# Kernel tuning notes

Measured on AMD Instinct MI355X. Metric: run time of the kernel, lower is better.

## Reference

```python
import jax, jax.numpy as jnp
import numpy as np

N_NODES = 100000
N_EDGES = 600000
IN_C, HID_C, OUT_C = 128, 128, 64


def setup_inputs() -> dict:
    key = jax.random.key(0)
    k1, k2, k3, k4 = jax.random.split(key, 4)
    x = jax.random.normal(k1, (N_NODES, IN_C), dtype=jnp.float32)
    edge_index = jax.random.randint(k2, (2, N_EDGES), 0, N_NODES, dtype=jnp.int64)
    # Glorot-ish init for linear weights
    W1 = jax.random.normal(k3, (IN_C, HID_C), dtype=jnp.float32) / np.sqrt(IN_C)
    b1 = jnp.zeros((HID_C,), dtype=jnp.float32)
    W2 = jax.random.normal(k4, (HID_C, OUT_C), dtype=jnp.float32) / np.sqrt(HID_C)
    b2 = jnp.zeros((OUT_C,), dtype=jnp.float32)
    prelu_a = jnp.full((1,), 0.25, dtype=jnp.float32)  # torch nn.PReLU default
    return {"x": x, "edge_index": edge_index, "W1": W1, "b1": b1,
            "W2": W2, "b2": b2, "prelu_a": prelu_a}


def _gcn_conv(x, src, dst, norm, W, b, num_nodes):
    # PyG GCNConv: h = x W; out[i] = sum_{(j->i)} norm_ji * h[j] + b
    h = x @ W                                   # [N, C_out]
    msg = h[src] * norm[:, None]                # [E', C_out] gather + scale
    out = jax.ops.segment_sum(msg, dst, num_segments=num_nodes)
    return out + b


def reference(x, edge_index, W1, b1, W2, b2, prelu_a):
    n = x.shape[0]
    # add self-loops
    loops = jnp.arange(n, dtype=edge_index.dtype)
    src = jnp.concatenate([edge_index[0], loops])
    dst = jnp.concatenate([edge_index[1], loops])
    # symmetric normalization deg^{-1/2}[src] * deg^{-1/2}[dst]
    deg = jax.ops.segment_sum(jnp.ones_like(dst, dtype=x.dtype), dst, num_segments=n)
    dinv = jnp.where(deg > 0, jax.lax.rsqrt(deg), 0.0)
    norm = dinv[src] * dinv[dst]
    # dropout p=0.0 -> identity
    h = _gcn_conv(x, src, dst, norm, W1, b1, n)
    h = jnp.where(h >= 0, h, prelu_a * h)       # PReLU (single shared parameter)
    out = _gcn_conv(h, src, dst, norm, W2, b2, n)
    return out
```

## Files before the change

### kernel.cpp

```cpp
#include <hip/hip_runtime.h>


typedef __attribute__((ext_vector_type(8))) short bf16x8;
typedef __attribute__((ext_vector_type(4))) float f32x4;

#define CAP 32

__device__ inline unsigned short f2bf(float f) {
    unsigned int b = __float_as_uint(f);
    b += 0x7FFFu + ((b >> 16) & 1u);
    return (unsigned short)(b >> 16);
}
__device__ inline float bflo(unsigned int u) { return __uint_as_float(u << 16); }
__device__ inline float bfhi(unsigned int u) { return __uint_as_float(u & 0xFFFF0000u); }

__global__ __launch_bounds__(512) void k_pre(
    const float* __restrict__ W1, const float* __restrict__ W2,
    unsigned short* __restrict__ Wt1, unsigned short* __restrict__ Wt2,
    const int* __restrict__ esrc, const int* __restrict__ edst,
    int* __restrict__ cnt, int* __restrict__ bucket, int ea) {
    const int t = blockIdx.x * 512 + threadIdx.x;
    if (t < 128 * 128) {
        int nn = t >> 7, k = t & 127;
        Wt1[t] = f2bf(W1[k * 128 + nn]);
    } else if (t < 128 * 128 + 64 * 128) {
        int j = t - 128 * 128;
        int nn = j >> 7, k = j & 127;
        Wt2[j] = f2bf(W2[k * 64 + nn]);
    }
    const int4* s4 = (const int4*)esrc;
    const int4* d4 = (const int4*)edst;
    for (int i = t; i < (ea >> 2); i += gridDim.x * 512) {
        int4 s = s4[i], d = d4[i];
        int p0 = atomicAdd(&cnt[d.x], 1);
        int p1 = atomicAdd(&cnt[d.y], 1);
        int p2 = atomicAdd(&cnt[d.z], 1);
        int p3 = atomicAdd(&cnt[d.w], 1);
        if (p0 < CAP) bucket[(size_t)d.x * CAP + p0] = s.x;
        if (p1 < CAP) bucket[(size_t)d.y * CAP + p1] = s.y;
        if (p2 < CAP) bucket[(size_t)d.z * CAP + p2] = s.z;
        if (p3 < CAP) bucket[(size_t)d.w * CAP + p3] = s.w;
    }
}

template <int BN, bool CVT, bool FILL>
__global__ __launch_bounds__(512) void k_gemm_mfma(
    const void* __restrict__ Asrc, const unsigned short* __restrict__ Wt,
    unsigned short* __restrict__ H, int n,
    const int* __restrict__ esrc, const int* __restrict__ edst,
    int* __restrict__ cnt, int* __restrict__ bucket, int e, int ea) {
    constexpr int PITCH = 136;
    __shared__ unsigned short Bs[BN * PITCH];
    const int tid = threadIdx.x;

    for (int q = tid; q < BN * 16; q += 512) {
        int row = q >> 4, c16 = q & 15;
        *(uint4*)(Bs + row * PITCH + c16 * 8) =
            *(const uint4*)(Wt + row * 128 + c16 * 8);
    }

    const int wave = tid >> 6, lane = tid & 63;
    const int ml = lane & 15;
    const int g = lane >> 4;
    const int stripe = blockIdx.x * 8 + wave;

    int ra = stripe * 16 + ml;
    if (ra >= n) ra = n - 1;

    bf16x8 af[4];
    if (CVT) {
        const float* A = (const float*)Asrc;
#pragma unroll
        for (int ks = 0; ks < 4; ++ks) {
            const float* p = A + (size_t)ra * 128 + ks * 32 + g * 8;
            float4 a0 = *(const float4*)p;
            float4 a1 = *(const float4*)(p + 4);
            uint4 pk;
            pk.x = (unsigned)f2bf(a0.x) | ((unsigned)f2bf(a0.y) << 16);
            pk.y = (unsigned)f2bf(a0.z) | ((unsigned)f2bf(a0.w) << 16);
            pk.z = (unsigned)f2bf(a1.x) | ((unsigned)f2bf(a1.y) << 16);
            pk.w = (unsigned)f2bf(a1.z) | ((unsigned)f2bf(a1.w) << 16);
            af[ks] = *(bf16x8*)&pk;
        }
    } else {
        const unsigned short* A = (const unsigned short*)Asrc;
#pragma unroll
        for (int ks = 0; ks < 4; ++ks)
            af[ks] = *(const bf16x8*)(A + (size_t)ra * 128 + ks * 32 + g * 8);
    }

    if (FILL) {
        for (int i = ea + blockIdx.x * 512 + tid; i < e; i += gridDim.x * 512) {
            int d = edst[i];
            int s = esrc[i];
            int pos = atomicAdd(&cnt[d], 1);
            if (pos < CAP) bucket[(size_t)d * CAP + pos] = s;
        }
    }

    __syncthreads();

    constexpr int NCT = BN / 16;
    f32x4 acc[NCT];
#pragma unroll
    for (int ct = 0; ct < NCT; ++ct) acc[ct] = (f32x4){0.f, 0.f, 0.f, 0.f};

#pragma unroll
    for (int ks = 0; ks < 4; ++ks)
#pragma unroll
        for (int ct = 0; ct < NCT; ++ct) {
            bf16x8 b = *(const bf16x8*)(Bs + (size_t)(ct * 16 + ml) * PITCH + ks * 32 + g * 8);
            acc[ct] = __builtin_amdgcn_mfma_f32_16x16x32_bf16(af[ks], b, acc[ct], 0, 0, 0);
        }

#pragma unroll
    for (int ct = 0; ct < NCT; ++ct)
#pragma unroll
        for (int reg = 0; reg < 4; ++reg) {
            int r = stripe * 16 + g * 4 + reg;
            if (r < n) H[(size_t)r * BN + ct * 16 + ml] = f2bf(acc[ct][reg]);
        }
}

__global__ __launch_bounds__(512) void k_gather_gemm(
    const unsigned short* __restrict__ H,
    const int* __restrict__ cnt, const int* __restrict__ bucket,
    const float* __restrict__ b1, const float* __restrict__ alpha_p,
    const unsigned short* __restrict__ Wt2,
    unsigned short* __restrict__ H2,
    int n) {
    constexpr int PITCH = 136;
    __shared__ unsigned short As[32 * PITCH];
    __shared__ unsigned short Bs[64 * PITCH];
    const int tid = threadIdx.x;

    for (int q = tid; q < 64 * 16; q += 512) {
        int row = q >> 4, c16 = q & 15;
        *(uint4*)(Bs + row * PITCH + c16 * 8) =
            *(const uint4*)(Wt2 + row * 128 + c16 * 8);
    }

    const int node = blockIdx.x * 32 + tid / 16;
    const int c0 = (tid & 15) * 8;
    const int lr = tid / 16;

    if (node < n) {
        int c = cnt[node];
        const float di = rsqrtf(1.0f + (float)c);
        if (c > CAP) c = CAP;

        float acc[8];
        {
            uint4 v = *(const uint4*)(H + (size_t)node * 128 + c0);
            float sl = di * di;
            acc[0] = bflo(v.x) * sl + b1[c0 + 0];
            acc[1] = bfhi(v.x) * sl + b1[c0 + 1];
            acc[2] = bflo(v.y) * sl + b1[c0 + 2];
            acc[3] = bfhi(v.y) * sl + b1[c0 + 3];
            acc[4] = bflo(v.z) * sl + b1[c0 + 4];
            acc[5] = bfhi(v.z) * sl + b1[c0 + 5];
            acc[6] = bflo(v.w) * sl + b1[c0 + 6];
            acc[7] = bfhi(v.w) * sl + b1[c0 + 7];
        }

        const int* bp = bucket + (size_t)node * CAP;
        const int nb4 = (c + 3) >> 2;
        for (int q = 0; q < nb4; ++q) {
            int4 idx = *(const int4*)(bp + q * 4);
            int base = q * 4;
            int s0 = idx.x;
            int s1 = (base + 1 < c) ? idx.y : s0;
            int s2 = (base + 2 < c) ? idx.z : s0;
            int s3 = (base + 3 < c) ? idx.w : s0;
            int cn0 = cnt[s0], cn1 = cnt[s1], cn2 = cnt[s2], cn3 = cnt[s3];
            uint4 v0 = *(const uint4*)(H + (size_t)s0 * 128 + c0);
            uint4 v1 = *(const uint4*)(H + (size_t)s1 * 128 + c0);
            uint4 v2 = *(const uint4*)(H + (size_t)s2 * 128 + c0);
            uint4 v3 = *(const uint4*)(H + (size_t)s3 * 128 + c0);
            float n0 = rsqrtf(1.0f + (float)cn0) * di;
            float n1 = (base + 1 < c) ? rsqrtf(1.0f + (float)cn1) * di : 0.0f;
            float n2 = (base + 2 < c) ? rsqrtf(1.0f + (float)cn2) * di : 0.0f;
            float n3 = (base + 3 < c) ? rsqrtf(1.0f + (float)cn3) * di : 0.0f;
            acc[0] += bflo(v0.x) * n0; acc[1] += bfhi(v0.x) * n0;
            acc[2] += bflo(v0.y) * n0; acc[3] += bfhi(v0.y) * n0;
            acc[4] += bflo(v0.z) * n0; acc[5] += bfhi(v0.z) * n0;
            acc[6] += bflo(v0.w) * n0; acc[7] += bfhi(v0.w) * n0;
            acc[0] += bflo(v1.x) * n1; acc[1] += bfhi(v1.x) * n1;
            acc[2] += bflo(v1.y) * n1; acc[3] += bfhi(v1.y) * n1;
            acc[4] += bflo(v1.z) * n1; acc[5] += bfhi(v1.z) * n1;
            acc[6] += bflo(v1.w) * n1; acc[7] += bfhi(v1.w) * n1;
            acc[0] += bflo(v2.x) * n2; acc[1] += bfhi(v2.x) * n2;
            acc[2] += bflo(v2.y) * n2; acc[3] += bfhi(v2.y) * n2;
            acc[4] += bflo(v2.z) * n2; acc[5] += bfhi(v2.z) * n2;
            acc[6] += bflo(v2.w) * n2; acc[7] += bfhi(v2.w) * n2;
            acc[0] += bflo(v3.x) * n3; acc[1] += bfhi(v3.x) * n3;
            acc[2] += bflo(v3.y) * n3; acc[3] += bfhi(v3.y) * n3;
            acc[4] += bflo(v3.z) * n3; acc[5] += bfhi(v3.z) * n3;
            acc[6] += bflo(v3.w) * n3; acc[7] += bfhi(v3.w) * n3;
        }

        float al = alpha_p[0];
        unsigned short o[8];
#pragma unroll
        for (int j = 0; j < 8; ++j) {
            float t = acc[j];
            t = (t >= 0.f) ? t : al * t;
            o[j] = f2bf(t);
        }
        uint4 pk;
        pk.x = (unsigned)o[0] | ((unsigned)o[1] << 16);
        pk.y = (unsigned)o[2] | ((unsigned)o[3] << 16);
        pk.z = (unsigned)o[4] | ((unsigned)o[5] << 16);
        pk.w = (unsigned)o[6] | ((unsigned)o[7] << 16);
        *(uint4*)(As + lr * PITCH + c0) = pk;
    }
    __syncthreads();

    const int wave = tid >> 6, lane = tid & 63;
    const int ml = lane & 15, g = lane >> 4;
    const int stripe = wave >> 2;
    const int ct = wave & 3;

    bf16x8 af[4];
#pragma unroll
    for (int ks = 0; ks < 4; ++ks)
        af[ks] = *(const bf16x8*)(As + (size_t)(stripe * 16 + ml) * PITCH + ks * 32 + g * 8);

    f32x4 acc2 = (f32x4){0.f, 0.f, 0.f, 0.f};
#pragma unroll
    for (int ks = 0; ks < 4; ++ks) {
        bf16x8 bb = *(const bf16x8*)(Bs + (size_t)(ct * 16 + ml) * PITCH + ks * 32 + g * 8);
        acc2 = __builtin_amdgcn_mfma_f32_16x16x32_bf16(af[ks], bb, acc2, 0, 0, 0);
    }

#pragma unroll
    for (int reg = 0; reg < 4; ++reg) {
        int r = blockIdx.x * 32 + stripe * 16 + g * 4 + reg;
        if (r < n) H2[(size_t)r * 64 + ct * 16 + ml] = f2bf(acc2[reg]);
    }
}

template <int COLS, bool PRELU_BF16_OUT>
__global__ void k_gather(const unsigned short* __restrict__ H,
                         const int* __restrict__ cnt, const int* __restrict__ bucket,
                         const float* __restrict__ b, void* __restrict__ outp,
                         const float* __restrict__ alpha_p, int n) {
    constexpr int NT = COLS / 8;
    constexpr int G = 256 / NT;
    const int tid = threadIdx.x;
    const int node = blockIdx.x * G + tid / NT;
    if (node >= n) return;
    const int c0 = (tid & (NT - 1)) * 8;

    int c = cnt[node];
    const float di = rsqrtf(1.0f + (float)c);
    if (c > CAP) c = CAP;

    float acc[8];
    {
        uint4 v = *(const uint4*)(H + (size_t)node * COLS + c0);
        float sl = di * di;
        acc[0] = bflo(v.x) * sl + b[c0 + 0];
        acc[1] = bfhi(v.x) * sl + b[c0 + 1];
        acc[2] = bflo(v.y) * sl + b[c0 + 2];
        acc[3] = bfhi(v.y) * sl + b[c0 + 3];
        acc[4] = bflo(v.z) * sl + b[c0 + 4];
        acc[5] = bfhi(v.z) * sl + b[c0 + 5];
        acc[6] = bflo(v.w) * sl + b[c0 + 6];
        acc[7] = bfhi(v.w) * sl + b[c0 + 7];
    }

    const int* bp = bucket + (size_t)node * CAP;
    const int nb4 = (c + 3) >> 2;
    for (int q = 0; q < nb4; ++q) {
        int4 idx = *(const int4*)(bp + q * 4);
        int base = q * 4;
        int s0 = idx.x;
        int s1 = (base + 1 < c) ? idx.y : s0;
        int s2 = (base + 2 < c) ? idx.z : s0;
        int s3 = (base + 3 < c) ? idx.w : s0;
        int cn0 = cnt[s0], cn1 = cnt[s1], cn2 = cnt[s2], cn3 = cnt[s3];
        uint4 v0 = *(const uint4*)(H + (size_t)s0 * COLS + c0);
        uint4 v1 = *(const uint4*)(H + (size_t)s1 * COLS + c0);
        uint4 v2 = *(const uint4*)(H + (size_t)s2 * COLS + c0);
        uint4 v3 = *(const uint4*)(H + (size_t)s3 * COLS + c0);
        float n0 = rsqrtf(1.0f + (float)cn0) * di;
        float n1 = (base + 1 < c) ? rsqrtf(1.0f + (float)cn1) * di : 0.0f;
        float n2 = (base + 2 < c) ? rsqrtf(1.0f + (float)cn2) * di : 0.0f;
        float n3 = (base + 3 < c) ? rsqrtf(1.0f + (float)cn3) * di : 0.0f;
        acc[0] += bflo(v0.x) * n0; acc[1] += bfhi(v0.x) * n0;
        acc[2] += bflo(v0.y) * n0; acc[3] += bfhi(v0.y) * n0;
        acc[4] += bflo(v0.z) * n0; acc[5] += bfhi(v0.z) * n0;
        acc[6] += bflo(v0.w) * n0; acc[7] += bfhi(v0.w) * n0;
        acc[0] += bflo(v1.x) * n1; acc[1] += bfhi(v1.x) * n1;
        acc[2] += bflo(v1.y) * n1; acc[3] += bfhi(v1.y) * n1;
        acc[4] += bflo(v1.z) * n1; acc[5] += bfhi(v1.z) * n1;
        acc[6] += bflo(v1.w) * n1; acc[7] += bfhi(v1.w) * n1;
        acc[0] += bflo(v2.x) * n2; acc[1] += bfhi(v2.x) * n2;
        acc[2] += bflo(v2.y) * n2; acc[3] += bfhi(v2.y) * n2;
        acc[4] += bflo(v2.z) * n2; acc[5] += bfhi(v2.z) * n2;
        acc[6] += bflo(v2.w) * n2; acc[7] += bfhi(v2.w) * n2;
        acc[0] += bflo(v3.x) * n3; acc[1] += bfhi(v3.x) * n3;
        acc[2] += bflo(v3.y) * n3; acc[3] += bfhi(v3.y) * n3;
        acc[4] += bflo(v3.z) * n3; acc[5] += bfhi(v3.z) * n3;
        acc[6] += bflo(v3.w) * n3; acc[7] += bfhi(v3.w) * n3;
    }

    if (PRELU_BF16_OUT) {
        float al = alpha_p[0];
        unsigned short o[8];
#pragma unroll
        for (int j = 0; j < 8; ++j) {
            float t = acc[j];
            t = (t >= 0.f) ? t : al * t;
            o[j] = f2bf(t);
        }
        uint4 pk;
        pk.x = (unsigned)o[0] | ((unsigned)o[1] << 16);
        pk.y = (unsigned)o[2] | ((unsigned)o[3] << 16);
        pk.z = (unsigned)o[4] | ((unsigned)o[5] << 16);
        pk.w = (unsigned)o[6] | ((unsigned)o[7] << 16);
        *(uint4*)((unsigned short*)outp + (size_t)node * COLS + c0) = pk;
    } else {
        float* out = (float*)outp;
        *(float4*)(out + (size_t)node * COLS + c0) =
            make_float4(acc[0], acc[1], acc[2], acc[3]);
        *(float4*)(out + (size_t)node * COLS + c0 + 4) =
            make_float4(acc[4], acc[5], acc[6], acc[7]);
    }
}

extern "C" void kernel_launch(void* const* d_in, const int* in_sizes, int n_in,
                              void* d_out, int out_size, void* d_ws, size_t ws_size,
                              hipStream_t stream) {
    const float* x  = (const float*)d_in[0];
    const int*   ei = (const int*)d_in[1];
    const float* W1 = (const float*)d_in[2];
    const float* b1 = (const float*)d_in[3];
    const float* W2 = (const float*)d_in[4];
    const float* b2 = (const float*)d_in[5];
    const float* pa = (const float*)d_in[6];
    float* out = (float*)d_out;

    const int n = in_sizes[0] / 128;
    const int e = in_sizes[1] / 2;
    const int* src = ei;
    const int* dst = ei + e;

    unsigned short* h1  = (unsigned short*)d_ws;
    unsigned short* h2  = h1 + (size_t)n * 128;
    unsigned short* Wt1 = h2 + (size_t)n * 64;
    unsigned short* Wt2 = Wt1 + 128 * 128;
    int* cnt     = (int*)(Wt2 + 64 * 128);
    int* bucket  = cnt + n;

    int EA = (int)(((long long)e * 7) / 10) & ~3;
    if ((e & 3) != 0) EA = 0;

    const int gblk = ((n + 15) / 16 + 7) / 8;
    int pblk = (EA / 4 + 511) / 512;
    if (pblk < 48) pblk = 48;

    hipMemsetAsync(cnt, 0, (size_t)n * sizeof(int), stream);
    k_pre<<<pblk, 512, 0, stream>>>(W1, W2, Wt1, Wt2, src, dst, cnt, bucket, EA);
    k_gemm_mfma<128, true, true><<<gblk, 512, 0, stream>>>(
        x, Wt1, h1, n, src, dst, cnt, bucket, e, EA);
    k_gather_gemm<<<(n + 31) / 32, 512, 0, stream>>>(h1, cnt, bucket, b1, pa,
                                                     Wt2, h2, n);
    k_gather<64, false><<<(n + 31) / 32, 256, 0, stream>>>(h2, cnt, bucket,
                                                           b2, out, nullptr, n);
}
```

Measured before the change: 190.3 us.

## Overlap edge bucketing with first GEMM and unroll gather neighbor loads

Replaces the memset plus split bucket fill with a prep kernel that converts weights and zeroes the counts. The whole edge bucketing now runs in 64 dedicated blocks of the first GEMM launch, so atomic scatter overlaps the MFMA GEMM blocks. Both gather kernels now issue the first eight neighbor loads up front for more memory-level parallelism, then loop over the rest in groups of four. This drops one launch and reduces per-kernel bucketing, but the edge work is concentrated in only 64 blocks, which may leave a long tail.

```diff
diff --git a/kernel.cpp b/kernel.cpp
--- a/kernel.cpp
+++ b/kernel.cpp
@@ -5,6 +5,7 @@
 typedef __attribute__((ext_vector_type(4))) float f32x4;
 
 #define CAP 32
+#define FB  64
 
 __device__ inline unsigned short f2bf(float f) {
     unsigned int b = __float_as_uint(f);
@@ -14,11 +15,17 @@
 __device__ inline float bflo(unsigned int u) { return __uint_as_float(u << 16); }
 __device__ inline float bfhi(unsigned int u) { return __uint_as_float(u & 0xFFFF0000u); }
 
-__global__ __launch_bounds__(512) void k_pre(
+__device__ inline void acc8(float* acc, uint4 v, float wgt) {
+    acc[0] += bflo(v.x) * wgt; acc[1] += bfhi(v.x) * wgt;
+    acc[2] += bflo(v.y) * wgt; acc[3] += bfhi(v.y) * wgt;
+    acc[4] += bflo(v.z) * wgt; acc[5] += bfhi(v.z) * wgt;
+    acc[6] += bflo(v.w) * wgt; acc[7] += bfhi(v.w) * wgt;
+}
+
+__global__ __launch_bounds__(512) void k_pre2(
     const float* __restrict__ W1, const float* __restrict__ W2,
     unsigned short* __restrict__ Wt1, unsigned short* __restrict__ Wt2,
-    const int* __restrict__ esrc, const int* __restrict__ edst,
-    int* __restrict__ cnt, int* __restrict__ bucket, int ea) {
+    int* __restrict__ cnt, int n) {
     const int t = blockIdx.x * 512 + threadIdx.x;
     if (t < 128 * 128) {
         int nn = t >> 7, k = t & 127;
@@ -28,32 +35,48 @@
         int nn = j >> 7, k = j & 127;
         Wt2[j] = f2bf(W2[k * 64 + nn]);
     }
-    const int4* s4 = (const int4*)esrc;
-    const int4* d4 = (const int4*)edst;
-    for (int i = t; i < (ea >> 2); i += gridDim.x * 512) {
-        int4 s = s4[i], d = d4[i];
-        int p0 = atomicAdd(&cnt[d.x], 1);
-        int p1 = atomicAdd(&cnt[d.y], 1);
-        int p2 = atomicAdd(&cnt[d.z], 1);
-        int p3 = atomicAdd(&cnt[d.w], 1);
-        if (p0 < CAP) bucket[(size_t)d.x * CAP + p0] = s.x;
-        if (p1 < CAP) bucket[(size_t)d.y * CAP + p1] = s.y;
-        if (p2 < CAP) bucket[(size_t)d.z * CAP + p2] = s.z;
-        if (p3 < CAP) bucket[(size_t)d.w * CAP + p3] = s.w;
-    }
-}
-
-template <int BN, bool CVT, bool FILL>
-__global__ __launch_bounds__(512) void k_gemm_mfma(
-    const void* __restrict__ Asrc, const unsigned short* __restrict__ Wt,
+    const int n4 = n >> 2;
+    for (int i = t; i < n4; i += gridDim.x * 512)
+        ((int4*)cnt)[i] = make_int4(0, 0, 0, 0);
+    if (blockIdx.x == 0 && threadIdx.x < (n & 3)) cnt[n4 * 4 + threadIdx.x] = 0;
+}
+
+__global__ __launch_bounds__(512) void k_conv1(
+    const float* __restrict__ x, const unsigned short* __restrict__ Wt,
     unsigned short* __restrict__ H, int n,
     const int* __restrict__ esrc, const int* __restrict__ edst,
-    int* __restrict__ cnt, int* __restrict__ bucket, int e, int ea) {
+    int* __restrict__ cnt, int* __restrict__ bucket, int e) {
     constexpr int PITCH = 136;
-    __shared__ unsigned short Bs[BN * PITCH];
+    __shared__ unsigned short Bs[128 * PITCH];
     const int tid = threadIdx.x;
 
-    for (int q = tid; q < BN * 16; q += 512) {
+    if (blockIdx.x < FB) {
+        const int t = blockIdx.x * 512 + tid;
+        const int e4 = e >> 2;
+        const int4* s4 = (const int4*)esrc;
+        const int4* d4 = (const int4*)edst;
+        for (int i = t; i < e4; i += FB * 512) {
+            int4 s = s4[i], d = d4[i];
+            int p0 = atomicAdd(&cnt[d.x], 1);
+            int p1 = atomicAdd(&cnt[d.y], 1);
+            int p2 = atomicAdd(&cnt[d.z], 1);
+            int p3 = atomicAdd(&cnt[d.w], 1);
+            if (p0 < CAP) bucket[(size_t)d.x * CAP + p0] = s.x;
+            if (p1 < CAP) bucket[(size_t)d.y * CAP + p1] = s.y;
+            if (p2 < CAP) bucket[(size_t)d.z * CAP + p2] = s.z;
+            if (p3 < CAP) bucket[(size_t)d.w * CAP + p3] = s.w;
+        }
+        if (blockIdx.x == 0 && tid < (e & 3)) {
+            int i = e4 * 4 + tid;
+            int d = edst[i], s = esrc[i];
+            int pos = atomicAdd(&cnt[d], 1);
+            if (pos < CAP) bucket[(size_t)d * CAP + pos] = s;
+        }
+        return;
+    }
+
+    const int bx = blockIdx.x - FB;
+    for (int q = tid; q < 128 * 16; q += 512) {
         int row = q >> 4, c16 = q & 15;
         *(uint4*)(Bs + row * PITCH + c16 * 8) =
             *(const uint4*)(Wt + row * 128 + c16 * 8);
@@ -62,63 +85,45 @@
     const int wave = tid >> 6, lane = tid & 63;
     const int ml = lane & 15;
     const int g = lane >> 4;
-    const int stripe = blockIdx.x * 8 + wave;
+    const int stripe = bx * 8 + wave;
 
     int ra = stripe * 16 + ml;
     if (ra >= n) ra = n - 1;
 
     bf16x8 af[4];
-    if (CVT) {
-        const float* A = (const float*)Asrc;
-#pragma unroll
-        for (int ks = 0; ks < 4; ++ks) {
-            const float* p = A + (size_t)ra * 128 + ks * 32 + g * 8;
-            float4 a0 = *(const float4*)p;
-            float4 a1 = *(const float4*)(p + 4);
-            uint4 pk;
-            pk.x = (unsigned)f2bf(a0.x) | ((unsigned)f2bf(a0.y) << 16);
-            pk.y = (unsigned)f2bf(a0.z) | ((unsigned)f2bf(a0.w) << 16);
-            pk.z = (unsigned)f2bf(a1.x) | ((unsigned)f2bf(a1.y) << 16);
-            pk.w = (unsigned)f2bf(a1.z) | ((unsigned)f2bf(a1.w) << 16);
-            af[ks] = *(bf16x8*)&pk;
-        }
-    } else {
-        const unsigned short* A = (const unsigned short*)Asrc;
-#pragma unroll
-        for (int ks = 0; ks < 4; ++ks)
-            af[ks] = *(const bf16x8*)(A + (size_t)ra * 128 + ks * 32 + g * 8);
-    }
-
-    if (FILL) {
-        for (int i = ea + blockIdx.x * 512 + tid; i < e; i += gridDim.x * 512) {
-            int d = edst[i];
-            int s = esrc[i];
-            int pos = atomicAdd(&cnt[d], 1);
-            if (pos < CAP) bucket[(size_t)d * CAP + pos] = s;
-        }
+#pragma unroll
+    for (int ks = 0; ks < 4; ++ks) {
+        const float* p = x + (size_t)ra * 128 + ks * 32 + g * 8;
+        float4 a0 = *(const float4*)p;
+        float4 a1 = *(const float4*)(p + 4);
+        uint4 pk;
+        pk.x = (unsigned)f2bf(a0.x) | ((unsigned)f2bf(a0.y) << 16);
+        pk.y = (unsigned)f2bf(a0.z) | ((unsigned)f2bf(a0.w) << 16);
+        pk.z = (unsigned)f2bf(a1.x) | ((unsigned)f2bf(a1.y) << 16);
+        pk.w = (unsigned)f2bf(a1.z) | ((unsigned)f2bf(a1.w) << 16);
+        af[ks] = *(bf16x8*)&pk;
     }
 
     __syncthreads();
 
-    constexpr int NCT = BN / 16;
-    f32x4 acc[NCT];
-#pragma unroll
-    for (int ct = 0; ct < NCT; ++ct) acc[ct] = (f32x4){0.f, 0.f, 0.f, 0.f};
+    f32x4 acc[8];
+#pragma unroll
+    for (int ct = 0; ct < 8; ++ct) acc[ct] = (f32x4){0.f, 0.f, 0.f, 0.f};
 
 #pragma unroll
     for (int ks = 0; ks < 4; ++ks)
 #pragma unroll
-        for (int ct = 0; ct < NCT; ++ct) {
+        for (int ct = 0; ct < 8; ++ct) {
             bf16x8 b = *(const bf16x8*)(Bs + (size_t)(ct * 16 + ml) * PITCH + ks * 32 + g * 8);
             acc[ct] = __builtin_amdgcn_mfma_f32_16x16x32_bf16(af[ks], b, acc[ct], 0, 0, 0);
         }
 
 #pragma unroll
-    for (int ct = 0; ct < NCT; ++ct)
+    for (int ct = 0; ct < 8; ++ct)
 #pragma unroll
         for (int reg = 0; reg < 4; ++reg) {
             int r = stripe * 16 + g * 4 + reg;
-            if (r < n) H[(size_t)r * BN + ct * 16 + ml] = f2bf(acc[ct][reg]);
+            if (r < n) H[(size_t)r * 128 + ct * 16 + ml] = f2bf(acc[ct][reg]);
         }
 }
 
@@ -163,40 +168,60 @@
             acc[7] = bfhi(v.w) * sl + b1[c0 + 7];
         }
 
-        const int* bp = bucket + (size_t)node * CAP;
-        const int nb4 = (c + 3) >> 2;
-        for (int q = 0; q < nb4; ++q) {
-            int4 idx = *(const int4*)(bp + q * 4);
-            int base = q * 4;
-            int s0 = idx.x;
-            int s1 = (base + 1 < c) ? idx.y : s0;
-            int s2 = (base + 2 < c) ? idx.z : s0;
-            int s3 = (base + 3 < c) ? idx.w : s0;
+        if (c > 0) {
+            const int* bp = bucket + (size_t)node * CAP;
+            int4 i0 = *(const int4*)bp;
+            int4 i1 = *(const int4*)(bp + 4);
+            int s0 = i0.x;
+            int s1 = (1 < c) ? i0.y : s0;
+            int s2 = (2 < c) ? i0.z : s0;
+            int s3 = (3 < c) ? i0.w : s0;
+            int s4 = (4 < c) ? i1.x : s0;
+            int s5 = (5 < c) ? i1.y : s0;
+            int s6 = (6 < c) ? i1.z : s0;
+            int s7 = (7 < c) ? i1.w : s0;
             int cn0 = cnt[s0], cn1 = cnt[s1], cn2 = cnt[s2], cn3 = cnt[s3];
+            int cn4 = cnt[s4], cn5 = cnt[s5], cn6 = cnt[s6], cn7 = cnt[s7];
             uint4 v0 = *(const uint4*)(H + (size_t)s0 * 128 + c0);
             uint4 v1 = *(const uint4*)(H + (size_t)s1 * 128 + c0);
             uint4 v2 = *(const uint4*)(H + (size_t)s2 * 128 + c0);
             uint4 v3 = *(const uint4*)(H + (size_t)s3 * 128 + c0);
-            float n0 = rsqrtf(1.0f + (float)cn0) * di;
-            float n1 = (base + 1 < c) ? rsqrtf(1.0f + (float)cn1) * di : 0.0f;
-            float n2 = (base + 2 < c) ? rsqrtf(1.0f + (float)cn2) * di : 0.0f;
-            float n3 = (base + 3 < c) ? rsqrtf(1.0f + (float)cn3) * di : 0.0f;
-            acc[0] += bflo(v0.x) * n0; acc[1] += bfhi(v0.x) * n0;
-            acc[2] += bflo(v0.y) * n0; acc[3] += bfhi(v0.y) * n0;
-            acc[4] += bflo(v0.z) * n0; acc[5] += bfhi(v0.z) * n0;
-            acc[6] += bflo(v0.w) * n0; acc[7] += bfhi(v0.w) * n0;
-            acc[0] += bflo(v1.x) * n1; acc[1] += bfhi(v1.x) * n1;
-            acc[2] += bflo(v1.y) * n1; acc[3] += bfhi(v1.y) * n1;
-            acc[4] += bflo(v1.z) * n1; acc[5] += bfhi(v1.z) * n1;
-            acc[6] += bflo(v1.w) * n1; acc[7] += bfhi(v1.w) * n1;
-            acc[0] += bflo(v2.x) * n2; acc[1] += bfhi(v2.x) * n2;
-            acc[2] += bflo(v2.y) * n2; acc[3] += bfhi(v2.y) * n2;
-            acc[4] += bflo(v2.z) * n2; acc[5] += bfhi(v2.z) * n2;
-            acc[6] += bflo(v2.w) * n2; acc[7] += bfhi(v2.w) * n2;
-            acc[0] += bflo(v3.x) * n3; acc[1] += bfhi(v3.x) * n3;
-            acc[2] += bflo(v3.y) * n3; acc[3] += bfhi(v3.y) * n3;
-            acc[4] += bflo(v3.z) * n3; acc[5] += bfhi(v3.z) * n3;
-            acc[6] += bflo(v3.w) * n3; acc[7] += bfhi(v3.w) * n3;
+            uint4 v4 = *(const uint4*)(H + (size_t)s4 * 128 + c0);
+            uint4 v5 = *(const uint4*)(H + (size_t)s5 * 128 + c0);
+            uint4 v6 = *(const uint4*)(H + (size_t)s6 * 128 + c0);
+            uint4 v7 = *(const uint4*)(H + (size_t)s7 * 128 + c0);
+            float w0 = rsqrtf(1.0f + (float)cn0) * di;
+            float w1 = (1 < c) ? rsqrtf(1.0f + (float)cn1) * di : 0.0f;
+            float w2 = (2 < c) ? rsqrtf(1.0f + (float)cn2) * di : 0.0f;
+            float w3 = (3 < c) ? rsqrtf(1.0f + (float)cn3) * di : 0.0f;
+            float w4 = (4 < c) ? rsqrtf(1.0f + (float)cn4) * di : 0.0f;
+            float w5 = (5 < c) ? rsqrtf(1.0f + (float)cn5) * di : 0.0f;
+            float w6 = (6 < c) ? rsqrtf(1.0f + (float)cn6) * di : 0.0f;
+            float w7 = (7 < c) ? rsqrtf(1.0f + (float)cn7) * di : 0.0f;
+            acc8(acc, v0, w0); acc8(acc, v1, w1);
+            acc8(acc, v2, w2); acc8(acc, v3, w3);
+            acc8(acc, v4, w4); acc8(acc, v5, w5);
+            acc8(acc, v6, w6); acc8(acc, v7, w7);
+
+            for (int q = 2; q * 4 < c; ++q) {
+                int4 idx = *(const int4*)(bp + q * 4);
+                int base = q * 4;
+                int t0 = idx.x;
+                int t1 = (base + 1 < c) ? idx.y : t0;
+                int t2 = (base + 2 < c) ? idx.z : t0;
+                int t3 = (base + 3 < c) ? idx.w : t0;
+                int d0 = cnt[t0], d1 = cnt[t1], d2 = cnt[t2], d3 = cnt[t3];
+                uint4 u0 = *(const uint4*)(H + (size_t)t0 * 128 + c0);
+                uint4 u1 = *(const uint4*)(H + (size_t)t1 * 128 + c0);
+                uint4 u2 = *(const uint4*)(H + (size_t)t2 * 128 + c0);
+                uint4 u3 = *(const uint4*)(H + (size_t)t3 * 128 + c0);
+                float y0 = rsqrtf(1.0f + (float)d0) * di;
+                float y1 = (base + 1 < c) ? rsqrtf(1.0f + (float)d1) * di : 0.0f;
+                float y2 = (base + 2 < c) ? rsqrtf(1.0f + (float)d2) * di : 0.0f;
+                float y3 = (base + 3 < c) ? rsqrtf(1.0f + (float)d3) * di : 0.0f;
+                acc8(acc, u0, y0); acc8(acc, u1, y1);
+                acc8(acc, u2, y2); acc8(acc, u3, y3);
+            }
         }
 
         float al = alpha_p[0];
@@ -240,11 +265,11 @@
     }
 }
 
-template <int COLS, bool PRELU_BF16_OUT>
-__global__ void k_gather(const unsigned short* __restrict__ H,
-                         const int* __restrict__ cnt, const int* __restrict__ bucket,
-                         const float* __restrict__ b, void* __restrict__ outp,
-                         const float* __restrict__ alpha_p, int n) {
+__global__ void k_gather2(const unsigned short* __restrict__ H,
+                          const int* __restrict__ cnt, const int* __restrict__ bucket,
+                          const float* __restrict__ b, float* __restrict__ out,
+                          int n) {
+    constexpr int COLS = 64;
     constexpr int NT = COLS / 8;
     constexpr int G = 256 / NT;
     const int tid = threadIdx.x;
@@ -270,64 +295,66 @@
         acc[7] = bfhi(v.w) * sl + b[c0 + 7];
     }
 
-    const int* bp = bucket + (size_t)node * CAP;
-    const int nb4 = (c + 3) >> 2;
-    for (int q = 0; q < nb4; ++q) {
-        int4 idx = *(const int4*)(bp + q * 4);
-        int base = q * 4;
-        int s0 = idx.x;
-        int s1 = (base + 1 < c) ? idx.y : s0;
-        int s2 = (base + 2 < c) ? idx.z : s0;
-        int s3 = (base + 3 < c) ? idx.w : s0;
+    if (c > 0) {
+        const int* bp = bucket + (size_t)node * CAP;
+        int4 i0 = *(const int4*)bp;
+        int4 i1 = *(const int4*)(bp + 4);
+        int s0 = i0.x;
+        int s1 = (1 < c) ? i0.y : s0;
+        int s2 = (2 < c) ? i0.z : s0;
+        int s3 = (3 < c) ? i0.w : s0;
+        int s4 = (4 < c) ? i1.x : s0;
+        int s5 = (5 < c) ? i1.y : s0;
+        int s6 = (6 < c) ? i1.z : s0;
+        int s7 = (7 < c) ? i1.w : s0;
         int cn0 = cnt[s0], cn1 = cnt[s1], cn2 = cnt[s2], cn3 = cnt[s3];
+        int cn4 = cnt[s4], cn5 = cnt[s5], cn6 = cnt[s6], cn7 = cnt[s7];
         uint4 v0 = *(const uint4*)(H + (size_t)s0 * COLS + c0);
         uint4 v1 = *(const uint4*)(H + (size_t)s1 * COLS + c0);
         uint4 v2 = *(const uint4*)(H + (size_t)s2 * COLS + c0);
         uint4 v3 = *(const uint4*)(H + (size_t)s3 * COLS + c0);
-        float n0 = rsqrtf(1.0f + (float)cn0) * di;
-        float n1 = (base + 1 < c) ? rsqrtf(1.0f + (float)cn1) * di : 0.0f;
-        float n2 = (base + 2 < c) ? rsqrtf(1.0f + (float)cn2) * di : 0.0f;
-        float n3 = (base + 3 < c) ? rsqrtf(1.0f + (float)cn3) * di : 0.0f;
-        acc[0] += bflo(v0.x) * n0; acc[1] += bfhi(v0.x) * n0;
-        acc[2] += bflo(v0.y) * n0; acc[3] += bfhi(v0.y) * n0;
-        acc[4] += bflo(v0.z) * n0; acc[5] += bfhi(v0.z) * n0;
-        acc[6] += bflo(v0.w) * n0; acc[7] += bfhi(v0.w) * n0;
-        acc[0] += bflo(v1.x) * n1; acc[1] += bfhi(v1.x) * n1;
-        acc[2] += bflo(v1.y) * n1; acc[3] += bfhi(v1.y) * n1;
-        acc[4] += bflo(v1.z) * n1; acc[5] += bfhi(v1.z) * n1;
-        acc[6] += bflo(v1.w) * n1; acc[7] += bfhi(v1.w) * n1;
-        acc[0] += bflo(v2.x) * n2; acc[1] += bfhi(v2.x) * n2;
-        acc[2] += bflo(v2.y) * n2; acc[3] += bfhi(v2.y) * n2;
-        acc[4] += bflo(v2.z) * n2; acc[5] += bfhi(v2.z) * n2;
-        acc[6] += bflo(v2.w) * n2; acc[7] += bfhi(v2.w) * n2;
-        acc[0] += bflo(v3.x) * n3; acc[1] += bfhi(v3.x) * n3;
-        acc[2] += bflo(v3.y) * n3; acc[3] += bfhi(v3.y) * n3;
-        acc[4] += bflo(v3.z) * n3; acc[5] += bfhi(v3.z) * n3;
-        acc[6] += bflo(v3.w) * n3; acc[7] += bfhi(v3.w) * n3;
-    }
-
-    if (PRELU_BF16_OUT) {
-        float al = alpha_p[0];
-        unsigned short o[8];
-#pragma unroll
-        for (int j = 0; j < 8; ++j) {
-            float t = acc[j];
-            t = (t >= 0.f) ? t : al * t;
-            o[j] = f2bf(t);
-        }
-        uint4 pk;
-        pk.x = (unsigned)o[0] | ((unsigned)o[1] << 16);
-        pk.y = (unsigned)o[2] | ((unsigned)o[3] << 16);
-        pk.z = (unsigned)o[4] | ((unsigned)o[5] << 16);
-        pk.w = (unsigned)o[6] | ((unsigned)o[7] << 16);
-        *(uint4*)((unsigned short*)outp + (size_t)node * COLS + c0) = pk;
-    } else {
-        float* out = (float*)outp;
-        *(float4*)(out + (size_t)node * COLS + c0) =
-            make_float4(acc[0], acc[1], acc[2], acc[3]);
-        *(float4*)(out + (size_t)node * COLS + c0 + 4) =
-            make_float4(acc[4], acc[5], acc[6], acc[7]);
-    }
+        uint4 v4 = *(const uint4*)(H + (size_t)s4 * COLS + c0);
+        uint4 v5 = *(const uint4*)(H + (size_t)s5 * COLS + c0);
+        uint4 v6 = *(const uint4*)(H + (size_t)s6 * COLS + c0);
+        uint4 v7 = *(const uint4*)(H + (size_t)s7 * COLS + c0);
+        float w0 = rsqrtf(1.0f + (float)cn0) * di;
+        float w1 = (1 < c) ? rsqrtf(1.0f + (float)cn1) * di : 0.0f;
+        float w2 = (2 < c) ? rsqrtf(1.0f + (float)cn2) * di : 0.0f;
+        float w3 = (3 < c) ? rsqrtf(1.0f + (float)cn3) * di : 0.0f;
+        float w4 = (4 < c) ? rsqrtf(1.0f + (float)cn4) * di : 0.0f;
+        float w5 = (5 < c) ? rsqrtf(1.0f + (float)cn5) * di : 0.0f;
+        float w6 = (6 < c) ? rsqrtf(1.0f + (float)cn6) * di : 0.0f;
+        float w7 = (7 < c) ? rsqrtf(1.0f + (float)cn7) * di : 0.0f;
+        acc8(acc, v0, w0); acc8(acc, v1, w1);
+        acc8(acc, v2, w2); acc8(acc, v3, w3);
+        acc8(acc, v4, w4); acc8(acc, v5, w5);
+        acc8(acc, v6, w6); acc8(acc, v7, w7);
+
+        for (int q = 2; q * 4 < c; ++q) {
+            int4 idx = *(const int4*)(bp + q * 4);
+            int base = q * 4;
+            int t0 = idx.x;
+            int t1 = (base + 1 < c) ? idx.y : t0;
+            int t2 = (base + 2 < c) ? idx.z : t0;
+            int t3 = (base + 3 < c) ? idx.w : t0;
+            int d0 = cnt[t0], d1 = cnt[t1], d2 = cnt[t2], d3 = cnt[t3];
+            uint4 u0 = *(const uint4*)(H + (size_t)t0 * COLS + c0);
+            uint4 u1 = *(const uint4*)(H + (size_t)t1 * COLS + c0);
+            uint4 u2 = *(const uint4*)(H + (size_t)t2 * COLS + c0);
+            uint4 u3 = *(const uint4*)(H + (size_t)t3 * COLS + c0);
+            float y0 = rsqrtf(1.0f + (float)d0) * di;
+            float y1 = (base + 1 < c) ? rsqrtf(1.0f + (float)d1) * di : 0.0f;
+            float y2 = (base + 2 < c) ? rsqrtf(1.0f + (float)d2) * di : 0.0f;
+            float y3 = (base + 3 < c) ? rsqrtf(1.0f + (float)d3) * di : 0.0f;
+            acc8(acc, u0, y0); acc8(acc, u1, y1);
+            acc8(acc, u2, y2); acc8(acc, u3, y3);
+        }
+    }
+
+    *(float4*)(out + (size_t)node * COLS + c0) =
+        make_float4(acc[0], acc[1], acc[2], acc[3]);
+    *(float4*)(out + (size_t)node * COLS + c0 + 4) =
+        make_float4(acc[4], acc[5], acc[6], acc[7]);
 }
 
 extern "C" void kernel_launch(void* const* d_in, const int* in_sizes, int n_in,
@@ -354,19 +381,12 @@
     int* cnt     = (int*)(Wt2 + 64 * 128);
     int* bucket  = cnt + n;
 
-    int EA = (int)(((long long)e * 7) / 10) & ~3;
-    if ((e & 3) != 0) EA = 0;
-
     const int gblk = ((n + 15) / 16 + 7) / 8;
-    int pblk = (EA / 4 + 511) / 512;
-    if (pblk < 48) pblk = 48;
-
-    hipMemsetAsync(cnt, 0, (size_t)n * sizeof(int), stream);
-    k_pre<<<pblk, 512, 0, stream>>>(W1, W2, Wt1, Wt2, src, dst, cnt, bucket, EA);
-    k_gemm_mfma<128, true, true><<<gblk, 512, 0, stream>>>(
-        x, Wt1, h1, n, src, dst, cnt, bucket, e, EA);
+
+    k_pre2<<<64, 512, 0, stream>>>(W1, W2, Wt1, Wt2, cnt, n);
+    k_conv1<<<FB + gblk, 512, 0, stream>>>(x, Wt1, h1, n, src, dst,
+                                           cnt, bucket, e);
     k_gather_gemm<<<(n + 31) / 32, 512, 0, stream>>>(h1, cnt, bucket, b1, pa,
                                                      Wt2, h2, n);
-    k_gather<64, false><<<(n + 31) / 32, 256, 0, stream>>>(h2, cnt, bucket,
-                                                           b2, out, nullptr, n);
-}
+    k_gather2<<<(n + 31) / 32, 256, 0, stream>>>(h2, cnt, bucket, b2, out, n);
+}
```

Result: slower. 201.3 us (+5.8%).
